# Performance work log

Measured on AMD Instinct MI355X. Metric: run time of the kernel, lower is better.

Reference implementation:

```python
import jax, jax.numpy as jnp
import numpy as np

H = 64          # h_dim
MSG = 64        # msg_dim
NUM_RBFS = 16
CUTOFF = 5.0
LN_EPS = 1e-5


def _gelu(v):
    # torch nn.GELU() default = exact erf gelu
    return jax.nn.gelu(v, approximate=False)


def setup_inputs() -> dict:
    key = jax.random.key(0)
    ks = jax.random.split(key, 24)

    def lin(k, din, dout):
        k1, k2 = jax.random.split(k)
        bound = 1.0 / np.sqrt(din)
        W = jax.random.uniform(k1, (din, dout), minval=-bound, maxval=bound, dtype=jnp.float32)
        b = jax.random.uniform(k2, (dout,), minval=-bound, maxval=bound, dtype=jnp.float32)
        return W, b

    B, N = 4, 512
    x = jax.random.normal(ks[0], (B, N, 3), dtype=jnp.float32)
    h = jax.random.normal(ks[1], (B, N, H), dtype=jnp.float32)
    node_mask = jnp.ones((B, N), dtype=bool)

    e_in_dim = 2 * H + NUM_RBFS
    e_w1, e_b1 = lin(ks[2], e_in_dim, MSG)
    e_w2, e_b2 = lin(ks[3], MSG, MSG)
    e_w3, e_b3 = lin(ks[4], MSG, MSG)
    n_w1, n_b1 = lin(ks[5], H + MSG, H)
    n_w2, n_b2 = lin(ks[6], H, H)
    n_w3, n_b3 = lin(ks[7], H, H)
    c_w1, c_b1 = lin(ks[8], MSG, MSG)
    c_w2, c_b2 = lin(ks[9], MSG, 1)
    ln_g = jnp.ones((H,), dtype=jnp.float32)
    ln_b = jnp.zeros((H,), dtype=jnp.float32)

    return dict(x=x, h=h, node_mask=node_mask,
                e_w1=e_w1, e_b1=e_b1, e_w2=e_w2, e_b2=e_b2, e_w3=e_w3, e_b3=e_b3,
                n_w1=n_w1, n_b1=n_b1, n_w2=n_w2, n_b2=n_b2, n_w3=n_w3, n_b3=n_b3,
                c_w1=c_w1, c_b1=c_b1, c_w2=c_w2, c_b2=c_b2,
                ln_g=ln_g, ln_b=ln_b)


def reference(x, h, node_mask,
              e_w1, e_b1, e_w2, e_b2, e_w3, e_b3,
              n_w1, n_b1, n_w2, n_b2, n_w3, n_b3,
              c_w1, c_b1, c_w2, c_b2,
              ln_g, ln_b):
    B, N, _ = x.shape
    mask = node_mask.astype(bool)

    # pairwise diffs / distances: (B,N,N,3), (B,N,N,1)
    dx = x[:, :, None, :] - x[:, None, :, :]
    dist2 = jnp.sum(dx * dx, axis=-1, keepdims=True)
    dist = jnp.sqrt(dist2 + 1e-8)

    self_mask = ~jnp.eye(N, dtype=bool)[None, :, :, None]
    mask_ij = (dist <= CUTOFF) & self_mask & mask[:, :, None, None] & mask[:, None, :, None]

    # Gaussian RBF expansion: (B,N,N,NUM_RBFS)
    centers = jnp.linspace(0.0, CUTOFF, NUM_RBFS, dtype=jnp.float32)
    gamma = jnp.float32((NUM_RBFS - 1) / CUTOFF)  # 1 / spacing
    rbf = jnp.exp(-0.5 * ((dist - centers) * gamma) ** 2)

    # edge features: (B,N,N,2H+R)
    hi = jnp.broadcast_to(h[:, :, None, :], (B, N, N, H))
    hj = jnp.broadcast_to(h[:, None, :, :], (B, N, N, H))
    e_in = jnp.concatenate([hi, hj, rbf], axis=-1)

    # edge MLP (2 hidden + out)
    m = _gelu(e_in @ e_w1 + e_b1)
    m = _gelu(m @ e_w2 + e_b2)
    m_ij = m @ e_w3 + e_b3
    m_ij = jnp.where(mask_ij, m_ij, 0.0)

    # aggregate messages: (B,N,MSG)
    m_i = jnp.sum(m_ij, axis=2)

    # node MLP + residual + LayerNorm
    u = _gelu(jnp.concatenate([h, m_i], axis=-1) @ n_w1 + n_b1)
    u = _gelu(u @ n_w2 + n_b2)
    h_up = u @ n_w3 + n_b3
    hr = h + h_up
    mu = jnp.mean(hr, axis=-1, keepdims=True)
    var = jnp.mean((hr - mu) ** 2, axis=-1, keepdims=True)
    h_new = (hr - mu) / jnp.sqrt(var + LN_EPS) * ln_g + ln_b

    # coord update: (B,N,N,1) gate
    g = _gelu(m_ij @ c_w1 + c_b1)
    g_ij = g @ c_w2 + c_b2
    g_ij = jnp.where(mask_ij, g_ij, 0.0)
    denom = jnp.clip(jnp.sum(mask_ij.astype(x.dtype), axis=2), 1.0, None)  # (B,N,1)
    delta = jnp.sum(dx * g_ij, axis=2) / denom
    x_new = x + delta

    nm = mask[:, :, None]
    x_new = jnp.where(nm, x_new, jax.lax.stop_gradient(x_new))
    h_new = jnp.where(nm, h_new, jax.lax.stop_gradient(h_new))
    return x_new, h_new
```

## Files before the change

kernel.cpp:

```cpp
#include <hip/hip_runtime.h>
#include <hip/hip_bf16.h>

#define NODES 2048
#define RS 68

typedef unsigned short ushort_t;
typedef __attribute__((ext_vector_type(8))) short short8;
typedef __attribute__((ext_vector_type(4))) float float4v;

#define LGKM0 asm volatile("s_waitcnt lgkmcnt(0)" ::: "memory")

__device__ __forceinline__ float fast_erf(float x){
    float ax = fabsf(x);
    float t  = __builtin_amdgcn_rcpf(fmaf(0.3275911f, ax, 1.0f));
    float p  = t * fmaf(t, fmaf(t, fmaf(t, fmaf(t, 1.061405429f, -1.453152027f),
                                        1.421413741f), -0.284496736f), 0.254829592f);
    float r  = 1.0f - p * __expf(-ax * ax);
    return copysignf(r, x);
}
__device__ __forceinline__ float gelu_f(float v){
    return 0.5f * v * (1.0f + fast_erf(v * 0.70710678f));
}
__device__ __forceinline__ ushort_t f2bf_hi(float f){
    union { float f; unsigned u; } v; v.f = f;
    unsigned r = v.u + 0x7fffu + ((v.u >> 16) & 1u);
    return (ushort_t)(r >> 16);
}
__device__ __forceinline__ float bfbits2f(ushort_t h){
    union { unsigned u; float f; } v; v.u = ((unsigned)h) << 16;
    return v.f;
}
__device__ __forceinline__ void split_bf_t(float f, ushort_t &hi, ushort_t &lo){
    hi = f2bf_hi(f);
    union { float f; unsigned u; } d; d.f = f - bfbits2f(hi);
    lo = (ushort_t)(d.u >> 16);
}

__global__ void node_pre_kernel(const float* __restrict__ hg,
                                const float* __restrict__ ew1,
                                const float* __restrict__ eb1,
                                float* __restrict__ a1, float* __restrict__ b1t){
    const int n = blockIdx.x, t = threadIdx.x;
    __shared__ float hs[64];
    hs[t] = hg[n * 64 + t];
    __syncthreads();
    float sa = 0.f;
    float sb = eb1[t];
    #pragma unroll
    for (int s = 0; s < 64; ++s){
        float hv = hs[s];
        sa = fmaf(hv, ew1[s * 64 + t], sa);
        sb = fmaf(hv, ew1[(64 + s) * 64 + t], sb);
    }
    a1[n * 64 + t] = sa;
    b1t[t * 2048 + n] = sb;
}

__global__ void wprep_kernel(const float* __restrict__ ew1, const float* __restrict__ ew2,
                             const float* __restrict__ ew3, const float* __restrict__ cw1,
                             ushort_t* __restrict__ wb){
    int idx = blockIdx.x * 256 + threadIdx.x;
    if (idx < 2048){
        int n = idx >> 5, k = idx & 31;
        float v = (k < 16) ? ew1[(128 + k) * 64 + n] : 0.f;
        ushort_t h, l; split_bf_t(v, h, l);
        wb[idx] = h; wb[2048 + idx] = l;
    } else if (idx < 14336){
        int t2 = idx - 2048;
        int which = t2 >> 12, r = t2 & 4095;
        int n = r >> 6, k = r & 63;
        const float* src = (which == 0) ? ew2 : (which == 1) ? ew3 : cw1;
        float v = src[k * 64 + n];
        ushort_t h, l; split_bf_t(v, h, l);
        ushort_t* H = wb + 4096 + which * 8192;
        H[r] = h; H[4096 + r] = l;
    }
}

#define MFMA1(ahh, bhh, accv) accv = __builtin_amdgcn_mfma_f32_16x16x32_bf16(ahh, bhh, accv, 0, 0, 0)
#define MFMA_NT(ntv, wHp, wLp, KS, kov, acc0v, acc1v) {                       \
    short8 bh = *(const short8*)((wHp) + ((ntv) * 16 + c) * (KS) + (kov));    \
    short8 bl = *(const short8*)((wLp) + ((ntv) * 16 + c) * (KS) + (kov));    \
    MFMA1(ah0, bh, acc0v); MFMA1(ah0, bl, acc0v);                             \
    MFMA1(ah1, bh, acc1v); MFMA1(ah1, bl, acc1v); }

#define MFMA_LAYER(NKT, KS, wHp, wLp)                                         \
  _Pragma("unroll")                                                           \
  for (int kt = 0; kt < (NKT); ++kt){                                         \
    const int ko = kt * 32 + q * 8;                                           \
    short8 ah0 = *(const short8*)(aH + (c     ) * RS + ko);                   \
    short8 ah1 = *(const short8*)(aH + (c + 16) * RS + ko);                   \
    MFMA_NT(0, wHp, wLp, KS, ko, acc00, acc10);                               \
    MFMA_NT(1, wHp, wLp, KS, ko, acc01, acc11);                               \
    MFMA_NT(2, wHp, wLp, KS, ko, acc02, acc12);                               \
    MFMA_NT(3, wHp, wLp, KS, ko, acc03, acc13);                               \
  }

#define MFMA_LAYER_GATE(wHp)                                                  \
  _Pragma("unroll")                                                           \
  for (int kt = 0; kt < 2; ++kt){                                             \
    const int ko = kt * 32 + q * 8;                                           \
    short8 ah0 = *(const short8*)(aH + (c     ) * RS + ko);                   \
    short8 ah1 = *(const short8*)(aH + (c + 16) * RS + ko);                   \
    { short8 bh = *(const short8*)((wHp) + (0 * 16 + c) * 64 + ko);           \
      MFMA1(ah0, bh, acc00); MFMA1(ah1, bh, acc10); }                         \
    { short8 bh = *(const short8*)((wHp) + (1 * 16 + c) * 64 + ko);           \
      MFMA1(ah0, bh, acc01); MFMA1(ah1, bh, acc11); }                         \
    { short8 bh = *(const short8*)((wHp) + (2 * 16 + c) * 64 + ko);           \
      MFMA1(ah0, bh, acc02); MFMA1(ah1, bh, acc12); }                         \
    { short8 bh = *(const short8*)((wHp) + (3 * 16 + c) * 64 + ko);           \
      MFMA1(ah0, bh, acc03); MFMA1(ah1, bh, acc13); }                         \
  }

#define ZERO_ACCS                                                             \
    acc00 = (float4v){0.f,0.f,0.f,0.f}; acc01 = (float4v){0.f,0.f,0.f,0.f};   \
    acc02 = (float4v){0.f,0.f,0.f,0.f}; acc03 = (float4v){0.f,0.f,0.f,0.f};   \
    acc10 = (float4v){0.f,0.f,0.f,0.f}; acc11 = (float4v){0.f,0.f,0.f,0.f};   \
    acc12 = (float4v){0.f,0.f,0.f,0.f}; acc13 = (float4v){0.f,0.f,0.f,0.f};

#define EPI1_NT(accv, ntv, mtv, bvv, a1s)                                     \
  _Pragma("unroll") for (int r = 0; r < 4; ++r){                              \
    const int mm = (mtv) * 16 + q * 4 + r;                                    \
    float gv = gelu_f(accv[r] + (a1s) + bvv[r]);                              \
    aH[mm * RS + (ntv) * 16 + c] = f2bf_hi(gv); }

#define EPI2_NT(accv, ntv, mtv, bs)                                           \
  _Pragma("unroll") for (int r = 0; r < 4; ++r){                              \
    const int mm = (mtv) * 16 + q * 4 + r;                                    \
    float gv = gelu_f(accv[r] + (bs));                                        \
    aH[mm * RS + (ntv) * 16 + c] = f2bf_hi(gv); }

#define EPI3_NT(accv, ntv, mtv, bs)                                           \
  _Pragma("unroll") for (int r = 0; r < 4; ++r){                              \
    const int mm = (mtv) * 16 + q * 4 + r;                                    \
    float v3 = (accv[r] + (bs)) * mk[(mtv) * 4 + r];                          \
    colp += v3;                                                               \
    aH[mm * RS + (ntv) * 16 + c] = f2bf_hi(v3); }

#define GATE_MT(A0v, A1v, A2v, A3v, mtv)                                      \
  _Pragma("unroll") for (int r = 0; r < 4; ++r){                              \
    float part = gelu_f(A0v[r] + cb1l0) * cw2l0                               \
               + gelu_f(A1v[r] + cb1l1) * cw2l1                               \
               + gelu_f(A2v[r] + cb1l2) * cw2l2                               \
               + gelu_f(A3v[r] + cb1l3) * cw2l3;                              \
    part += __shfl_xor(part, 1, 64);                                          \
    part += __shfl_xor(part, 2, 64);                                          \
    part += __shfl_xor(part, 4, 64);                                          \
    part += __shfl_xor(part, 8, 64);                                          \
    const int mm = (mtv) * 16 + q * 4 + r;                                    \
    if (c == 0) ed[mm * 5 + 4] = mk[(mtv) * 4 + r] * (cb2v + part); }

__launch_bounds__(256, 4)
__global__ void edge_kernel(const float* __restrict__ xg, const float* __restrict__ hg,
                            const float* __restrict__ eb2g, const float* __restrict__ eb3g,
                            const float* __restrict__ cb1g, const float* __restrict__ cw2g,
                            const float* __restrict__ cb2g,
                            const float* __restrict__ nw1, const float* __restrict__ nb1,
                            const float* __restrict__ nw2, const float* __restrict__ nb2,
                            const float* __restrict__ nw3, const float* __restrict__ nb3,
                            const float* __restrict__ lng, const float* __restrict__ lnb,
                            const float* __restrict__ a1g, const float* __restrict__ b1t,
                            const ushort_t* __restrict__ wb,
                            float* __restrict__ out){
    __shared__ ushort_t actH[4][32 * RS];
    __shared__ float edat[4][32 * 5];
    __shared__ float miw[4][64];
    __shared__ float hi_s[64], mi_s[64], ubA[64], ubB[64];
    __shared__ float cred[4][4];

    const int tid  = threadIdx.x;
    const int w    = tid >> 6, lane = tid & 63;
    const int c    = lane & 15, q = lane >> 4;
    const int node = blockIdx.x, b = node >> 9, i = node & 511;
    const int nodeOff = node * 64;

    if (tid < 64) hi_s[tid] = hg[nodeOff + tid];

    const float xi0 = xg[node * 3 + 0];
    const float xi1 = xg[node * 3 + 1];
    const float xi2 = xg[node * 3 + 2];
    const float cb2v = cb2g[0];

    ushort_t* aH = actH[w];
    float* ed = edat[w];

    float dsx = 0.f, dsy = 0.f, dsz = 0.f, cntf = 0.f;
    float miv[4] = {0.f, 0.f, 0.f, 0.f};

    #pragma unroll 1
    for (int g = 0; g < 4; ++g){
        const int jbase = (w * 4 + g) * 32;
        const int jn0   = b * 512 + jbase;

        const ushort_t *w1h = wb,         *w1l = wb + 2048;
        const ushort_t *w2h = wb + 4096,  *w2l = wb + 8192;
        const ushort_t *w3h = wb + 12288, *w3l = wb + 16384;
        const ushort_t *wch = wb + 20480;
        const float *peb2 = eb2g, *peb3 = eb3g;
        const float *pcb1 = cb1g, *pcw2 = cw2g;
        asm volatile("" : "+s"(w1h), "+s"(w1l), "+s"(w2h), "+s"(w2l),
                          "+s"(w3h), "+s"(w3l), "+s"(wch),
                          "+s"(peb2), "+s"(peb3), "+s"(pcb1), "+s"(pcw2));

        {
            const int e = lane & 31, half = lane >> 5;
            const int j = jbase + e, jn = b * 512 + j;
            float xj0 = xg[jn * 3 + 0], xj1 = xg[jn * 3 + 1], xj2 = xg[jn * 3 + 2];
            float d0 = xi0 - xj0, d1 = xi1 - xj1, d2 = xi2 - xj2;
            float dist2 = __fadd_rn(__fadd_rn(__fmul_rn(d0,d0), __fmul_rn(d1,d1)), __fmul_rn(d2,d2));
            float dist  = sqrtf(__fadd_rn(dist2, 1e-8f));
            float maskf = (dist <= 5.0f && j != i) ? 1.0f : 0.0f;
            #pragma unroll
            for (int p = 0; p < 4; ++p){
                int k0 = half * 8 + 2 * p;
                float t0 = (dist - (float)k0 * (5.0f / 15.0f)) * 3.0f;
                float t1 = (dist - (float)(k0 + 1) * (5.0f / 15.0f)) * 3.0f;
                float r0 = __expf(-0.5f * t0 * t0);
                float r1 = __expf(-0.5f * t1 * t1);
                *(unsigned*)(aH + e * RS + k0) =
                    (unsigned)f2bf_hi(r0) | ((unsigned)f2bf_hi(r1) << 16);
            }
            short8 z8 = (short8){0,0,0,0,0,0,0,0};
            *(short8*)(aH + e * RS + 16 + half * 8) = z8;
            if (half == 0){
                ed[e * 5 + 0] = maskf; ed[e * 5 + 1] = d0;
                ed[e * 5 + 2] = d1;    ed[e * 5 + 3] = d2;
            }
        }

        float4v acc00, acc01, acc02, acc03, acc10, acc11, acc12, acc13;

        ZERO_ACCS;
        MFMA_LAYER(1, 32, w1h, w1l);
        {
            const float *pb1 = b1t, *pa1 = a1g;
            asm volatile("" : "+s"(pb1), "+s"(pa1));
            float4v bv00 = *(const float4v*)(pb1 + (0 * 16 + c) * 2048 + jn0 +  0 + q * 4);
            float4v bv01 = *(const float4v*)(pb1 + (1 * 16 + c) * 2048 + jn0 +  0 + q * 4);
            float4v bv02 = *(const float4v*)(pb1 + (2 * 16 + c) * 2048 + jn0 +  0 + q * 4);
            float4v bv03 = *(const float4v*)(pb1 + (3 * 16 + c) * 2048 + jn0 +  0 + q * 4);
            float4v bv10 = *(const float4v*)(pb1 + (0 * 16 + c) * 2048 + jn0 + 16 + q * 4);
            float4v bv11 = *(const float4v*)(pb1 + (1 * 16 + c) * 2048 + jn0 + 16 + q * 4);
            float4v bv12 = *(const float4v*)(pb1 + (2 * 16 + c) * 2048 + jn0 + 16 + q * 4);
            float4v bv13 = *(const float4v*)(pb1 + (3 * 16 + c) * 2048 + jn0 + 16 + q * 4);
            float a1l0 = pa1[nodeOff + c];
            float a1l1 = pa1[nodeOff + 16 + c];
            float a1l2 = pa1[nodeOff + 32 + c];
            float a1l3 = pa1[nodeOff + 48 + c];
            EPI1_NT(acc00, 0, 0, bv00, a1l0); EPI1_NT(acc01, 1, 0, bv01, a1l1);
            EPI1_NT(acc02, 2, 0, bv02, a1l2); EPI1_NT(acc03, 3, 0, bv03, a1l3);
            EPI1_NT(acc10, 0, 1, bv10, a1l0); EPI1_NT(acc11, 1, 1, bv11, a1l1);
            EPI1_NT(acc12, 2, 1, bv12, a1l2); EPI1_NT(acc13, 3, 1, bv13, a1l3);
        }

        ZERO_ACCS;
        {
            MFMA_LAYER(2, 64, w2h, w2l);
            float eb2l0 = peb2[c], eb2l1 = peb2[16 + c], eb2l2 = peb2[32 + c], eb2l3 = peb2[48 + c];
            EPI2_NT(acc00, 0, 0, eb2l0); EPI2_NT(acc01, 1, 0, eb2l1);
            EPI2_NT(acc02, 2, 0, eb2l2); EPI2_NT(acc03, 3, 0, eb2l3);
            EPI2_NT(acc10, 0, 1, eb2l0); EPI2_NT(acc11, 1, 1, eb2l1);
            EPI2_NT(acc12, 2, 1, eb2l2); EPI2_NT(acc13, 3, 1, eb2l3);
        }

        float mk[8];
        ZERO_ACCS;
        {
            MFMA_LAYER(2, 64, w3h, w3l);
            float eb3l0 = peb3[c], eb3l1 = peb3[16 + c], eb3l2 = peb3[32 + c], eb3l3 = peb3[48 + c];
            #pragma unroll
            for (int mt = 0; mt < 2; ++mt)
                #pragma unroll
                for (int r = 0; r < 4; ++r) mk[mt * 4 + r] = ed[(mt * 16 + q * 4 + r) * 5];
            { float colp = 0.f; EPI3_NT(acc00, 0, 0, eb3l0); EPI3_NT(acc10, 0, 1, eb3l0);
              colp += __shfl_xor(colp, 16, 64); colp += __shfl_xor(colp, 32, 64); miv[0] += colp; }
            { float colp = 0.f; EPI3_NT(acc01, 1, 0, eb3l1); EPI3_NT(acc11, 1, 1, eb3l1);
              colp += __shfl_xor(colp, 16, 64); colp += __shfl_xor(colp, 32, 64); miv[1] += colp; }
            { float colp = 0.f; EPI3_NT(acc02, 2, 0, eb3l2); EPI3_NT(acc12, 2, 1, eb3l2);
              colp += __shfl_xor(colp, 16, 64); colp += __shfl_xor(colp, 32, 64); miv[2] += colp; }
            { float colp = 0.f; EPI3_NT(acc03, 3, 0, eb3l3); EPI3_NT(acc13, 3, 1, eb3l3);
              colp += __shfl_xor(colp, 16, 64); colp += __shfl_xor(colp, 32, 64); miv[3] += colp; }
        }

        ZERO_ACCS;
        {
            MFMA_LAYER_GATE(wch);
            float cb1l0 = pcb1[c], cb1l1 = pcb1[16 + c], cb1l2 = pcb1[32 + c], cb1l3 = pcb1[48 + c];
            float cw2l0 = pcw2[c], cw2l1 = pcw2[16 + c], cw2l2 = pcw2[32 + c], cw2l3 = pcw2[48 + c];
            GATE_MT(acc00, acc01, acc02, acc03, 0);
            GATE_MT(acc10, acc11, acc12, acc13, 1);
        }

        if (lane < 32){
            const int e = lane;
            float gv = ed[e * 5 + 4];
            dsx = fmaf(gv, ed[e * 5 + 1], dsx);
            dsy = fmaf(gv, ed[e * 5 + 2], dsy);
            dsz = fmaf(gv, ed[e * 5 + 3], dsz);
            cntf += ed[e * 5 + 0];
        }
    }

    #pragma unroll
    for (int m2 = 1; m2 < 32; m2 <<= 1){
        dsx  += __shfl_xor(dsx,  m2, 64);
        dsy  += __shfl_xor(dsy,  m2, 64);
        dsz  += __shfl_xor(dsz,  m2, 64);
        cntf += __shfl_xor(cntf, m2, 64);
    }
    if (lane == 0){
        cred[w][0] = dsx; cred[w][1] = dsy; cred[w][2] = dsz; cred[w][3] = cntf;
    }
    if (q == 0){
        #pragma unroll
        for (int nt = 0; nt < 4; ++nt) miw[w][nt * 16 + c] = miv[nt];
    }
    __syncthreads();

    if (tid < 64){
        const int t = tid;
        mi_s[t] = miw[0][t] + miw[1][t] + miw[2][t] + miw[3][t];
        if (t < 3){
            float td = cred[0][t] + cred[1][t] + cred[2][t] + cred[3][t];
            float tc = cred[0][3] + cred[1][3] + cred[2][3] + cred[3][3];
            out[node * 3 + t] = xg[node * 3 + t] + td / fmaxf(tc, 1.0f);
        }
        LGKM0;

        float s1 = nb1[t];
        for (int s = 0; s < 64; ++s) s1 = fmaf(hi_s[s], nw1[s * 64 + t], s1);
        for (int s = 0; s < 64; ++s) s1 = fmaf(mi_s[s], nw1[(64 + s) * 64 + t], s1);
        ubA[t] = gelu_f(s1);
        LGKM0;
        float s2 = nb2[t];
        for (int s = 0; s < 64; ++s) s2 = fmaf(ubA[s], nw2[s * 64 + t], s2);
        ubB[t] = gelu_f(s2);
        LGKM0;
        float s3 = nb3[t];
        for (int s = 0; s < 64; ++s) s3 = fmaf(ubB[s], nw3[s * 64 + t], s3);
        float hr = hi_s[t] + s3;

        float sum = hr;
        #pragma unroll
        for (int m2 = 1; m2 < 64; m2 <<= 1) sum += __shfl_xor(sum, m2, 64);
        float mu = sum * (1.0f / 64.0f);
        float dv = hr - mu;
        float vs = dv * dv;
        #pragma unroll
        for (int m2 = 1; m2 < 64; m2 <<= 1) vs += __shfl_xor(vs, m2, 64);
        float var = vs * (1.0f / 64.0f);
        float hn = dv / sqrtf(var + 1e-5f) * lng[t] + lnb[t];
        out[6144 + node * 64 + t] = hn;
    }
}

extern "C" void kernel_launch(void* const* d_in, const int* in_sizes, int n_in,
                              void* d_out, int out_size, void* d_ws, size_t ws_size,
                              hipStream_t stream){
    const float* x   = (const float*)d_in[0];
    const float* h   = (const float*)d_in[1];
    const float* ew1 = (const float*)d_in[3];
    const float* eb1 = (const float*)d_in[4];
    const float* ew2 = (const float*)d_in[5];
    const float* eb2 = (const float*)d_in[6];
    const float* ew3 = (const float*)d_in[7];
    const float* eb3 = (const float*)d_in[8];
    const float* nw1 = (const float*)d_in[9];
    const float* nb1 = (const float*)d_in[10];
    const float* nw2 = (const float*)d_in[11];
    const float* nb2 = (const float*)d_in[12];
    const float* nw3 = (const float*)d_in[13];
    const float* nb3 = (const float*)d_in[14];
    const float* cw1 = (const float*)d_in[15];
    const float* cb1 = (const float*)d_in[16];
    const float* cw2 = (const float*)d_in[17];
    const float* cb2 = (const float*)d_in[18];
    const float* lng = (const float*)d_in[19];
    const float* lnb = (const float*)d_in[20];

    float* a1  = (float*)d_ws;
    float* b1t = a1 + 2048 * 64;
    ushort_t* wb = (ushort_t*)(b1t + 64 * 2048);
    float* out = (float*)d_out;

    wprep_kernel<<<56, 256, 0, stream>>>(ew1, ew2, ew3, cw1, wb);
    node_pre_kernel<<<NODES, 64, 0, stream>>>(h, ew1, eb1, a1, b1t);
    edge_kernel<<<NODES, 256, 0, stream>>>(x, h, eb2, eb3, cb1, cw2, cb2,
                                           nw1, nb1, nw2, nb2, nw3, nb3,
                                           lng, lnb, a1, b1t, wb, out);
}
```

Measured before the change: 336.0 us.

## Transpose edge MLP MFMA operands so epilogues vectorize bf16 stores

```diff
diff --git a/kernel.cpp b/kernel.cpp
--- a/kernel.cpp
+++ b/kernel.cpp
@@ -7,6 +7,7 @@
 typedef unsigned short ushort_t;
 typedef __attribute__((ext_vector_type(8))) short short8;
 typedef __attribute__((ext_vector_type(4))) float float4v;
+typedef __attribute__((ext_vector_type(2))) unsigned uint2v;
 
 #define LGKM0 asm volatile("s_waitcnt lgkmcnt(0)" ::: "memory")
 
@@ -18,8 +19,13 @@
     float r  = 1.0f - p * __expf(-ax * ax);
     return copysignf(r, x);
 }
-__device__ __forceinline__ float gelu_f(float v){
+__device__ __forceinline__ float gelu_x(float v){
     return 0.5f * v * (1.0f + fast_erf(v * 0.70710678f));
+}
+__device__ __forceinline__ unsigned cvt_pk_bf16(float a, float b){
+    unsigned r;
+    asm("v_cvt_pk_bf16_f32 %0, %1, %2" : "=v"(r) : "v"(a), "v"(b));
+    return r;
 }
 __device__ __forceinline__ ushort_t f2bf_hi(float f){
     union { float f; unsigned u; } v; v.f = f;
@@ -39,7 +45,7 @@
 __global__ void node_pre_kernel(const float* __restrict__ hg,
                                 const float* __restrict__ ew1,
                                 const float* __restrict__ eb1,
-                                float* __restrict__ a1, float* __restrict__ b1t){
+                                float* __restrict__ a1, float* __restrict__ b1n){
     const int n = blockIdx.x, t = threadIdx.x;
     __shared__ float hs[64];
     hs[t] = hg[n * 64 + t];
@@ -53,7 +59,7 @@
         sb = fmaf(hv, ew1[(64 + s) * 64 + t], sb);
     }
     a1[n * 64 + t] = sa;
-    b1t[t * 2048 + n] = sb;
+    b1n[n * 64 + t] = sb;
 }
 
 __global__ void wprep_kernel(const float* __restrict__ ew1, const float* __restrict__ ew2,
@@ -77,78 +83,88 @@
     }
 }
 
-#define MFMA1(ahh, bhh, accv) accv = __builtin_amdgcn_mfma_f32_16x16x32_bf16(ahh, bhh, accv, 0, 0, 0)
-#define MFMA_NT(ntv, wHp, wLp, KS, kov, acc0v, acc1v) {                       \
-    short8 bh = *(const short8*)((wHp) + ((ntv) * 16 + c) * (KS) + (kov));    \
-    short8 bl = *(const short8*)((wLp) + ((ntv) * 16 + c) * (KS) + (kov));    \
-    MFMA1(ah0, bh, acc0v); MFMA1(ah0, bl, acc0v);                             \
-    MFMA1(ah1, bh, acc1v); MFMA1(ah1, bl, acc1v); }
-
-#define MFMA_LAYER(NKT, KS, wHp, wLp)                                         \
+#define MFMA1(av, bv, accv) accv = __builtin_amdgcn_mfma_f32_16x16x32_bf16(av, bv, accv, 0, 0, 0)
+
+#define MFMA_MT(mtv, wHp, wLp, KS, kov, accN0, accN1) {                       \
+    short8 wh = *(const short8*)((wHp) + ((mtv) * 16 + c) * (KS) + (kov));    \
+    short8 wl = *(const short8*)((wLp) + ((mtv) * 16 + c) * (KS) + (kov));    \
+    MFMA1(wh, bh0, accN0); MFMA1(wl, bh0, accN0);                             \
+    MFMA1(wh, bh1, accN1); MFMA1(wl, bh1, accN1); }
+
+#define MFMA_LAYER_T(NKT, KS, wHp, wLp)                                       \
   _Pragma("unroll")                                                           \
   for (int kt = 0; kt < (NKT); ++kt){                                         \
     const int ko = kt * 32 + q * 8;                                           \
-    short8 ah0 = *(const short8*)(aH + (c     ) * RS + ko);                   \
-    short8 ah1 = *(const short8*)(aH + (c + 16) * RS + ko);                   \
-    MFMA_NT(0, wHp, wLp, KS, ko, acc00, acc10);                               \
-    MFMA_NT(1, wHp, wLp, KS, ko, acc01, acc11);                               \
-    MFMA_NT(2, wHp, wLp, KS, ko, acc02, acc12);                               \
-    MFMA_NT(3, wHp, wLp, KS, ko, acc03, acc13);                               \
+    short8 bh0 = *(const short8*)(aH + (c     ) * RS + ko);                   \
+    short8 bh1 = *(const short8*)(aH + (c + 16) * RS + ko);                   \
+    MFMA_MT(0, wHp, wLp, KS, ko, acc00, acc01);                               \
+    MFMA_MT(1, wHp, wLp, KS, ko, acc10, acc11);                               \
+    MFMA_MT(2, wHp, wLp, KS, ko, acc20, acc21);                               \
+    MFMA_MT(3, wHp, wLp, KS, ko, acc30, acc31);                               \
   }
 
-#define MFMA_LAYER_GATE(wHp)                                                  \
+#define MFMA_GATE_T(wHp)                                                      \
   _Pragma("unroll")                                                           \
   for (int kt = 0; kt < 2; ++kt){                                             \
     const int ko = kt * 32 + q * 8;                                           \
-    short8 ah0 = *(const short8*)(aH + (c     ) * RS + ko);                   \
-    short8 ah1 = *(const short8*)(aH + (c + 16) * RS + ko);                   \
-    { short8 bh = *(const short8*)((wHp) + (0 * 16 + c) * 64 + ko);           \
-      MFMA1(ah0, bh, acc00); MFMA1(ah1, bh, acc10); }                         \
-    { short8 bh = *(const short8*)((wHp) + (1 * 16 + c) * 64 + ko);           \
-      MFMA1(ah0, bh, acc01); MFMA1(ah1, bh, acc11); }                         \
-    { short8 bh = *(const short8*)((wHp) + (2 * 16 + c) * 64 + ko);           \
-      MFMA1(ah0, bh, acc02); MFMA1(ah1, bh, acc12); }                         \
-    { short8 bh = *(const short8*)((wHp) + (3 * 16 + c) * 64 + ko);           \
-      MFMA1(ah0, bh, acc03); MFMA1(ah1, bh, acc13); }                         \
+    short8 bh0 = *(const short8*)(aH + (c     ) * RS + ko);                   \
+    short8 bh1 = *(const short8*)(aH + (c + 16) * RS + ko);                   \
+    { short8 wh = *(const short8*)((wHp) + (0 * 16 + c) * 64 + ko);           \
+      MFMA1(wh, bh0, acc00); MFMA1(wh, bh1, acc01); }                         \
+    { short8 wh = *(const short8*)((wHp) + (1 * 16 + c) * 64 + ko);           \
+      MFMA1(wh, bh0, acc10); MFMA1(wh, bh1, acc11); }                         \
+    { short8 wh = *(const short8*)((wHp) + (2 * 16 + c) * 64 + ko);           \
+      MFMA1(wh, bh0, acc20); MFMA1(wh, bh1, acc21); }                         \
+    { short8 wh = *(const short8*)((wHp) + (3 * 16 + c) * 64 + ko);           \
+      MFMA1(wh, bh0, acc30); MFMA1(wh, bh1, acc31); }                         \
   }
 
 #define ZERO_ACCS                                                             \
     acc00 = (float4v){0.f,0.f,0.f,0.f}; acc01 = (float4v){0.f,0.f,0.f,0.f};   \
-    acc02 = (float4v){0.f,0.f,0.f,0.f}; acc03 = (float4v){0.f,0.f,0.f,0.f};   \
     acc10 = (float4v){0.f,0.f,0.f,0.f}; acc11 = (float4v){0.f,0.f,0.f,0.f};   \
-    acc12 = (float4v){0.f,0.f,0.f,0.f}; acc13 = (float4v){0.f,0.f,0.f,0.f};
-
-#define EPI1_NT(accv, ntv, mtv, bvv, a1s)                                     \
-  _Pragma("unroll") for (int r = 0; r < 4; ++r){                              \
-    const int mm = (mtv) * 16 + q * 4 + r;                                    \
-    float gv = gelu_f(accv[r] + (a1s) + bvv[r]);                              \
-    aH[mm * RS + (ntv) * 16 + c] = f2bf_hi(gv); }
-
-#define EPI2_NT(accv, ntv, mtv, bs)                                           \
-  _Pragma("unroll") for (int r = 0; r < 4; ++r){                              \
-    const int mm = (mtv) * 16 + q * 4 + r;                                    \
-    float gv = gelu_f(accv[r] + (bs));                                        \
-    aH[mm * RS + (ntv) * 16 + c] = f2bf_hi(gv); }
-
-#define EPI3_NT(accv, ntv, mtv, bs)                                           \
-  _Pragma("unroll") for (int r = 0; r < 4; ++r){                              \
-    const int mm = (mtv) * 16 + q * 4 + r;                                    \
-    float v3 = (accv[r] + (bs)) * mk[(mtv) * 4 + r];                          \
-    colp += v3;                                                               \
-    aH[mm * RS + (ntv) * 16 + c] = f2bf_hi(v3); }
-
-#define GATE_MT(A0v, A1v, A2v, A3v, mtv)                                      \
-  _Pragma("unroll") for (int r = 0; r < 4; ++r){                              \
-    float part = gelu_f(A0v[r] + cb1l0) * cw2l0                               \
-               + gelu_f(A1v[r] + cb1l1) * cw2l1                               \
-               + gelu_f(A2v[r] + cb1l2) * cw2l2                               \
-               + gelu_f(A3v[r] + cb1l3) * cw2l3;                              \
-    part += __shfl_xor(part, 1, 64);                                          \
-    part += __shfl_xor(part, 2, 64);                                          \
-    part += __shfl_xor(part, 4, 64);                                          \
-    part += __shfl_xor(part, 8, 64);                                          \
-    const int mm = (mtv) * 16 + q * 4 + r;                                    \
-    if (c == 0) ed[mm * 5 + 4] = mk[(mtv) * 4 + r] * (cb2v + part); }
+    acc20 = (float4v){0.f,0.f,0.f,0.f}; acc21 = (float4v){0.f,0.f,0.f,0.f};   \
+    acc30 = (float4v){0.f,0.f,0.f,0.f}; acc31 = (float4v){0.f,0.f,0.f,0.f};
+
+#define STORE4(g0, g1, g2, g3, mtv, ntv) {                                    \
+    uint2v pk_; pk_.x = cvt_pk_bf16(g0, g1); pk_.y = cvt_pk_bf16(g2, g3);     \
+    *(uint2v*)(aH + ((ntv) * 16 + c) * RS + (mtv) * 16 + q * 4) = pk_; }
+
+#define EPI1_MT(acc0v, acc1v, mtv) {                                          \
+    float4v av  = *(const float4v*)(pa1 + nodeOff + (mtv) * 16 + q * 4);      \
+    float4v bv0 = *(const float4v*)(pb1 + (jn0 +      c) * 64 + (mtv) * 16 + q * 4); \
+    float4v bv1 = *(const float4v*)(pb1 + (jn0 + 16 + c) * 64 + (mtv) * 16 + q * 4); \
+    STORE4(gelu_x(acc0v[0] + av[0] + bv0[0]), gelu_x(acc0v[1] + av[1] + bv0[1]),     \
+           gelu_x(acc0v[2] + av[2] + bv0[2]), gelu_x(acc0v[3] + av[3] + bv0[3]), mtv, 0); \
+    STORE4(gelu_x(acc1v[0] + av[0] + bv1[0]), gelu_x(acc1v[1] + av[1] + bv1[1]),     \
+           gelu_x(acc1v[2] + av[2] + bv1[2]), gelu_x(acc1v[3] + av[3] + bv1[3]), mtv, 1); }
+
+#define EPI2_MT(acc0v, acc1v, mtv) {                                          \
+    float4v bvv = *(const float4v*)(peb2 + (mtv) * 16 + q * 4);               \
+    STORE4(gelu_x(acc0v[0] + bvv[0]), gelu_x(acc0v[1] + bvv[1]),              \
+           gelu_x(acc0v[2] + bvv[2]), gelu_x(acc0v[3] + bvv[3]), mtv, 0);     \
+    STORE4(gelu_x(acc1v[0] + bvv[0]), gelu_x(acc1v[1] + bvv[1]),              \
+           gelu_x(acc1v[2] + bvv[2]), gelu_x(acc1v[3] + bvv[3]), mtv, 1); }
+
+#define EPI3_MT(acc0v, acc1v, mtv) {                                          \
+    float4v bvv = *(const float4v*)(peb3 + (mtv) * 16 + q * 4);               \
+    float v0 = (acc0v[0] + bvv[0]) * mk0, v1 = (acc0v[1] + bvv[1]) * mk0;     \
+    float v2 = (acc0v[2] + bvv[2]) * mk0, v3 = (acc0v[3] + bvv[3]) * mk0;     \
+    STORE4(v0, v1, v2, v3, mtv, 0);                                          \
+    v0 = (acc1v[0] + bvv[0]) * mk1; v1 = (acc1v[1] + bvv[1]) * mk1;           \
+    v2 = (acc1v[2] + bvv[2]) * mk1; v3 = (acc1v[3] + bvv[3]) * mk1;           \
+    STORE4(v0, v1, v2, v3, mtv, 1); }
+
+#define GATE_MT_T(acc0v, acc1v, mtv) {                                        \
+    float4v c1v = *(const float4v*)(pcb1 + (mtv) * 16 + q * 4);               \
+    float4v w2v = *(const float4v*)(pcw2 + (mtv) * 16 + q * 4);               \
+    pg0 = fmaf(gelu_x(acc0v[0] + c1v[0]), w2v[0], pg0);                       \
+    pg0 = fmaf(gelu_x(acc0v[1] + c1v[1]), w2v[1], pg0);                       \
+    pg0 = fmaf(gelu_x(acc0v[2] + c1v[2]), w2v[2], pg0);                       \
+    pg0 = fmaf(gelu_x(acc0v[3] + c1v[3]), w2v[3], pg0);                       \
+    pg1 = fmaf(gelu_x(acc1v[0] + c1v[0]), w2v[0], pg1);                       \
+    pg1 = fmaf(gelu_x(acc1v[1] + c1v[1]), w2v[1], pg1);                       \
+    pg1 = fmaf(gelu_x(acc1v[2] + c1v[2]), w2v[2], pg1);                       \
+    pg1 = fmaf(gelu_x(acc1v[3] + c1v[3]), w2v[3], pg1); }
 
 __launch_bounds__(256, 4)
 __global__ void edge_kernel(const float* __restrict__ xg, const float* __restrict__ hg,
@@ -159,7 +175,7 @@
                             const float* __restrict__ nw2, const float* __restrict__ nb2,
                             const float* __restrict__ nw3, const float* __restrict__ nb3,
                             const float* __restrict__ lng, const float* __restrict__ lnb,
-                            const float* __restrict__ a1g, const float* __restrict__ b1t,
+                            const float* __restrict__ a1g, const float* __restrict__ b1ng,
                             const ushort_t* __restrict__ wb,
                             float* __restrict__ out){
     __shared__ ushort_t actH[4][32 * RS];
@@ -185,7 +201,7 @@
     float* ed = edat[w];
 
     float dsx = 0.f, dsy = 0.f, dsz = 0.f, cntf = 0.f;
-    float miv[4] = {0.f, 0.f, 0.f, 0.f};
+    float macc0 = 0.f, macc1 = 0.f;
 
     #pragma unroll 1
     for (int g = 0; g < 4; ++g){
@@ -217,8 +233,7 @@
                 float t1 = (dist - (float)(k0 + 1) * (5.0f / 15.0f)) * 3.0f;
                 float r0 = __expf(-0.5f * t0 * t0);
                 float r1 = __expf(-0.5f * t1 * t1);
-                *(unsigned*)(aH + e * RS + k0) =
-                    (unsigned)f2bf_hi(r0) | ((unsigned)f2bf_hi(r1) << 16);
+                *(unsigned*)(aH + e * RS + k0) = cvt_pk_bf16(r0, r1);
             }
             short8 z8 = (short8){0,0,0,0,0,0,0,0};
             *(short8*)(aH + e * RS + 16 + half * 8) = z8;
@@ -228,67 +243,68 @@
             }
         }
 
-        float4v acc00, acc01, acc02, acc03, acc10, acc11, acc12, acc13;
+        const float mk0 = ed[c * 5];
+        const float mk1 = ed[(16 + c) * 5];
+
+        float4v acc00, acc01, acc10, acc11, acc20, acc21, acc30, acc31;
 
         ZERO_ACCS;
-        MFMA_LAYER(1, 32, w1h, w1l);
-        {
-            const float *pb1 = b1t, *pa1 = a1g;
+        MFMA_LAYER_T(1, 32, w1h, w1l);
+        {
+            const float *pb1 = b1ng, *pa1 = a1g;
             asm volatile("" : "+s"(pb1), "+s"(pa1));
-            float4v bv00 = *(const float4v*)(pb1 + (0 * 16 + c) * 2048 + jn0 +  0 + q * 4);
-            float4v bv01 = *(const float4v*)(pb1 + (1 * 16 + c) * 2048 + jn0 +  0 + q * 4);
-            float4v bv02 = *(const float4v*)(pb1 + (2 * 16 + c) * 2048 + jn0 +  0 + q * 4);
-            float4v bv03 = *(const float4v*)(pb1 + (3 * 16 + c) * 2048 + jn0 +  0 + q * 4);
-            float4v bv10 = *(const float4v*)(pb1 + (0 * 16 + c) * 2048 + jn0 + 16 + q * 4);
-            float4v bv11 = *(const float4v*)(pb1 + (1 * 16 + c) * 2048 + jn0 + 16 + q * 4);
-            float4v bv12 = *(const float4v*)(pb1 + (2 * 16 + c) * 2048 + jn0 + 16 + q * 4);
-            float4v bv13 = *(const float4v*)(pb1 + (3 * 16 + c) * 2048 + jn0 + 16 + q * 4);
-            float a1l0 = pa1[nodeOff + c];
-            float a1l1 = pa1[nodeOff + 16 + c];
-            float a1l2 = pa1[nodeOff + 32 + c];
-            float a1l3 = pa1[nodeOff + 48 + c];
-            EPI1_NT(acc00, 0, 0, bv00, a1l0); EPI1_NT(acc01, 1, 0, bv01, a1l1);
-            EPI1_NT(acc02, 2, 0, bv02, a1l2); EPI1_NT(acc03, 3, 0, bv03, a1l3);
-            EPI1_NT(acc10, 0, 1, bv10, a1l0); EPI1_NT(acc11, 1, 1, bv11, a1l1);
-            EPI1_NT(acc12, 2, 1, bv12, a1l2); EPI1_NT(acc13, 3, 1, bv13, a1l3);
+            EPI1_MT(acc00, acc01, 0);
+            EPI1_MT(acc10, acc11, 1);
+            EPI1_MT(acc20, acc21, 2);
+            EPI1_MT(acc30, acc31, 3);
         }
 
         ZERO_ACCS;
         {
-            MFMA_LAYER(2, 64, w2h, w2l);
-            float eb2l0 = peb2[c], eb2l1 = peb2[16 + c], eb2l2 = peb2[32 + c], eb2l3 = peb2[48 + c];
-            EPI2_NT(acc00, 0, 0, eb2l0); EPI2_NT(acc01, 1, 0, eb2l1);
-            EPI2_NT(acc02, 2, 0, eb2l2); EPI2_NT(acc03, 3, 0, eb2l3);
-            EPI2_NT(acc10, 0, 1, eb2l0); EPI2_NT(acc11, 1, 1, eb2l1);
-            EPI2_NT(acc12, 2, 1, eb2l2); EPI2_NT(acc13, 3, 1, eb2l3);
-        }
-
-        float mk[8];
+            MFMA_LAYER_T(2, 64, w2h, w2l);
+            EPI2_MT(acc00, acc01, 0);
+            EPI2_MT(acc10, acc11, 1);
+            EPI2_MT(acc20, acc21, 2);
+            EPI2_MT(acc30, acc31, 3);
+        }
+
         ZERO_ACCS;
         {
-            MFMA_LAYER(2, 64, w3h, w3l);
-            float eb3l0 = peb3[c], eb3l1 = peb3[16 + c], eb3l2 = peb3[32 + c], eb3l3 = peb3[48 + c];
+            MFMA_LAYER_T(2, 64, w3h, w3l);
+            EPI3_MT(acc00, acc01, 0);
+            EPI3_MT(acc10, acc11, 1);
+            EPI3_MT(acc20, acc21, 2);
+            EPI3_MT(acc30, acc31, 3);
+        }
+
+        {
+            const int fp = (lane & 31) * 2;
+            const int e0 = (lane >> 5) * 16;
             #pragma unroll
-            for (int mt = 0; mt < 2; ++mt)
-                #pragma unroll
-                for (int r = 0; r < 4; ++r) mk[mt * 4 + r] = ed[(mt * 16 + q * 4 + r) * 5];
-            { float colp = 0.f; EPI3_NT(acc00, 0, 0, eb3l0); EPI3_NT(acc10, 0, 1, eb3l0);
-              colp += __shfl_xor(colp, 16, 64); colp += __shfl_xor(colp, 32, 64); miv[0] += colp; }
-            { float colp = 0.f; EPI3_NT(acc01, 1, 0, eb3l1); EPI3_NT(acc11, 1, 1, eb3l1);
-              colp += __shfl_xor(colp, 16, 64); colp += __shfl_xor(colp, 32, 64); miv[1] += colp; }
-            { float colp = 0.f; EPI3_NT(acc02, 2, 0, eb3l2); EPI3_NT(acc12, 2, 1, eb3l2);
-              colp += __shfl_xor(colp, 16, 64); colp += __shfl_xor(colp, 32, 64); miv[2] += colp; }
-            { float colp = 0.f; EPI3_NT(acc03, 3, 0, eb3l3); EPI3_NT(acc13, 3, 1, eb3l3);
-              colp += __shfl_xor(colp, 16, 64); colp += __shfl_xor(colp, 32, 64); miv[3] += colp; }
+            for (int e = 0; e < 16; ++e){
+                unsigned u = *(const unsigned*)(aH + (e0 + e) * RS + fp);
+                union { unsigned u; float f; } lo, hi;
+                lo.u = u << 16; hi.u = u & 0xffff0000u;
+                macc0 += lo.f; macc1 += hi.f;
+            }
         }
 
         ZERO_ACCS;
         {
-            MFMA_LAYER_GATE(wch);
-            float cb1l0 = pcb1[c], cb1l1 = pcb1[16 + c], cb1l2 = pcb1[32 + c], cb1l3 = pcb1[48 + c];
-            float cw2l0 = pcw2[c], cw2l1 = pcw2[16 + c], cw2l2 = pcw2[32 + c], cw2l3 = pcw2[48 + c];
-            GATE_MT(acc00, acc01, acc02, acc03, 0);
-            GATE_MT(acc10, acc11, acc12, acc13, 1);
+            MFMA_GATE_T(wch);
+            float pg0 = 0.f, pg1 = 0.f;
+            GATE_MT_T(acc00, acc01, 0);
+            GATE_MT_T(acc10, acc11, 1);
+            GATE_MT_T(acc20, acc21, 2);
+            GATE_MT_T(acc30, acc31, 3);
+            pg0 += __shfl_xor(pg0, 16, 64);
+            pg0 += __shfl_xor(pg0, 32, 64);
+            pg1 += __shfl_xor(pg1, 16, 64);
+            pg1 += __shfl_xor(pg1, 32, 64);
+            if (q == 0){
+                ed[c * 5 + 4]        = mk0 * (cb2v + pg0);
+                ed[(16 + c) * 5 + 4] = mk1 * (cb2v + pg1);
+            }
         }
 
         if (lane < 32){
@@ -311,9 +327,11 @@
     if (lane == 0){
         cred[w][0] = dsx; cred[w][1] = dsy; cred[w][2] = dsz; cred[w][3] = cntf;
     }
-    if (q == 0){
-        #pragma unroll
-        for (int nt = 0; nt < 4; ++nt) miw[w][nt * 16 + c] = miv[nt];
+    macc0 += __shfl_xor(macc0, 32, 64);
+    macc1 += __shfl_xor(macc1, 32, 64);
+    if (lane < 32){
+        miw[w][(lane & 31) * 2]     = macc0;
+        miw[w][(lane & 31) * 2 + 1] = macc1;
     }
     __syncthreads();
 
@@ -330,11 +348,11 @@
         float s1 = nb1[t];
         for (int s = 0; s < 64; ++s) s1 = fmaf(hi_s[s], nw1[s * 64 + t], s1);
         for (int s = 0; s < 64; ++s) s1 = fmaf(mi_s[s], nw1[(64 + s) * 64 + t], s1);
-        ubA[t] = gelu_f(s1);
+        ubA[t] = gelu_x(s1);
         LGKM0;
         float s2 = nb2[t];
         for (int s = 0; s < 64; ++s) s2 = fmaf(ubA[s], nw2[s * 64 + t], s2);
-        ubB[t] = gelu_f(s2);
+        ubB[t] = gelu_x(s2);
         LGKM0;
         float s3 = nb3[t];
         for (int s = 0; s < 64; ++s) s3 = fmaf(ubB[s], nw3[s * 64 + t], s3);
@@ -379,13 +397,13 @@
     const float* lnb = (const float*)d_in[20];
 
     float* a1  = (float*)d_ws;
-    float* b1t = a1 + 2048 * 64;
-    ushort_t* wb = (ushort_t*)(b1t + 64 * 2048);
+    float* b1n = a1 + 2048 * 64;
+    ushort_t* wb = (ushort_t*)(b1n + 64 * 2048);
     float* out = (float*)d_out;
 
     wprep_kernel<<<56, 256, 0, stream>>>(ew1, ew2, ew3, cw1, wb);
-    node_pre_kernel<<<NODES, 64, 0, stream>>>(h, ew1, eb1, a1, b1t);
+    node_pre_kernel<<<NODES, 64, 0, stream>>>(h, ew1, eb1, a1, b1n);
     edge_kernel<<<NODES, 256, 0, stream>>>(x, h, eb2, eb3, cb1, cw2, cb2,
                                            nw1, nb1, nw2, nb2, nw3, nb3,
-                                           lng, lnb, a1, b1t, wb, out);
-}
+                                           lng, lnb, a1, b1n, wb, out);
+}
```

Result: faster. 322.4 us (-4.0%).
